# Performance work log

Hardware: AMD Instinct MI355X
Metric: run time of the kernel (lower is better)

The kernel has to match this reference:

```python
import jax, jax.numpy as jnp
import numpy as np

D_MODEL = 1024
N_HEADS = 16
DIM_HEAD = D_MODEL // N_HEADS
SCALE = DIM_HEAD ** -0.5


def setup_inputs() -> dict:
    key = jax.random.key(0)
    ks = jax.random.split(key, 7)
    B, N = 2, 2048
    q = jax.random.normal(ks[0], (B, N, D_MODEL), dtype=jnp.float32)
    # boolean mask: True = masked out; keep sparse so softmax rows stay valid
    mask = jax.random.bernoulli(ks[1], 0.1, (B, N, N))
    s = D_MODEL ** -0.5
    Wq = jax.random.normal(ks[2], (D_MODEL, D_MODEL), dtype=jnp.float32) * s
    Wk = jax.random.normal(ks[3], (D_MODEL, D_MODEL), dtype=jnp.float32) * s
    Wv = jax.random.normal(ks[4], (D_MODEL, D_MODEL), dtype=jnp.float32) * s
    Wo = jax.random.normal(ks[5], (D_MODEL, D_MODEL), dtype=jnp.float32) * s
    bo = jnp.zeros((D_MODEL,), dtype=jnp.float32)
    return {"q": q, "mask": mask, "Wq": Wq, "Wk": Wk, "Wv": Wv, "Wo": Wo, "bo": bo}


def reference(q, mask, Wq, Wk, Wv, Wo, bo):
    B, N, D = q.shape
    # self-attention: memory = q. nn.Linear applies x @ W.T (W is [out, in]).
    qh = (q @ Wq.T) * SCALE
    kh = q @ Wk.T
    vh = q @ Wv.T
    # b n (h d) -> b h n d
    qh = qh.reshape(B, N, N_HEADS, DIM_HEAD).transpose(0, 2, 1, 3)
    kh = kh.reshape(B, N, N_HEADS, DIM_HEAD).transpose(0, 2, 1, 3)
    vh = vh.reshape(B, N, N_HEADS, DIM_HEAD).transpose(0, 2, 1, 3)
    scores = jnp.einsum('bhid,bhjd->bhij', qh, kh)  # [B,H,N,N]
    mask_value = -jnp.finfo(scores.dtype).max
    scores = jnp.where(mask[:, None, :, :], mask_value, scores)
    attn = jax.nn.softmax(scores, axis=-1)
    o = jnp.einsum('bhij,bhjd->bhid', attn, vh)
    o = o.transpose(0, 2, 1, 3).reshape(B, N, D)  # b h n d -> b n (h d)
    return o @ Wo.T + bo
```

## Files before the change

kernel.cpp:

```cpp
#include <hip/hip_runtime.h>
#include <hip/hip_bf16.h>

typedef float fx4 __attribute__((ext_vector_type(4)));
typedef short s16x8 __attribute__((ext_vector_type(8)));

#define NSEQ 2048
#define DM   1024
#define NH   16
#define DH   64
#define MROWS 4096
#define NWORDS (2 * NSEQ * (NSEQ / 64))

#define QK_SCALE (0.125f * 1.44269504088896f)

__device__ __forceinline__ unsigned short f2bf(float f) {
    union { float f; unsigned u; } c; c.f = f;
    unsigned u = c.u;
    unsigned r = u + 0x7FFFu + ((u >> 16) & 1u);
    return (unsigned short)(r >> 16);
}

__device__ __forceinline__ float exp2_fast(float x) {
#if __has_builtin(__builtin_amdgcn_exp2f)
    return __builtin_amdgcn_exp2f(x);
#else
    return exp2f(x);
#endif
}

__device__ __forceinline__ unsigned cvt_pk_bf16(float a, float b) {
    unsigned r;
    asm("v_cvt_pk_bf16_f32 %0, %1, %2" : "=v"(r) : "v"(a), "v"(b));
    return r;
}

__device__ __forceinline__ fx4 zero4() {
    fx4 z; z[0] = 0.f; z[1] = 0.f; z[2] = 0.f; z[3] = 0.f; return z;
}

__device__ __forceinline__ void gload16(const void* g, void* l) {
    __builtin_amdgcn_global_load_lds(
        (const __attribute__((address_space(1))) unsigned int*)g,
        (__attribute__((address_space(3))) unsigned int*)l,
        16, 0, 0);
}

__global__ void cvt_kernel(const float* __restrict__ in,
                           unsigned short* __restrict__ out, int n4) {
    int i = blockIdx.x * blockDim.x + threadIdx.x;
    if (i >= n4) return;
    float4 v = reinterpret_cast<const float4*>(in)[i];
    ushort4 o;
    o.x = f2bf(v.x); o.y = f2bf(v.y); o.z = f2bf(v.z); o.w = f2bf(v.w);
    reinterpret_cast<ushort4*>(out)[i] = o;
}

__global__ void cvt4_kernel(const float* __restrict__ w0, const float* __restrict__ w1,
                            const float* __restrict__ w2, const float* __restrict__ w3,
                            unsigned short* __restrict__ o0, unsigned short* __restrict__ o1,
                            unsigned short* __restrict__ o2, unsigned short* __restrict__ o3) {
    const float* in; unsigned short* out;
    switch (blockIdx.y) {
        case 0:  in = w0; out = o0; break;
        case 1:  in = w1; out = o1; break;
        case 2:  in = w2; out = o2; break;
        default: in = w3; out = o3; break;
    }
    int i = blockIdx.x * blockDim.x + threadIdx.x;
    float4 v = reinterpret_cast<const float4*>(in)[i];
    ushort4 o;
    o.x = f2bf(v.x); o.y = f2bf(v.y); o.z = f2bf(v.z); o.w = f2bf(v.w);
    reinterpret_cast<ushort4*>(out)[i] = o;
}

__global__ void mask_detect(const unsigned int* __restrict__ m, int* __restrict__ flag) {
    unsigned mx = 0;
    int stride = gridDim.x * blockDim.x;
    for (int i = blockIdx.x * blockDim.x + threadIdx.x; i < (2 * NSEQ * NSEQ) / 4; i += stride) {
        unsigned v = m[i];
        mx = v > mx ? v : mx;
    }
    if (__any(mx > 1u)) {
        if ((threadIdx.x & 63) == 0) atomicOr(flag, 1);
    }
}

__global__ void mask_pack(const void* __restrict__ mask, const int* __restrict__ mflag,
                          unsigned long long* __restrict__ packed) {
    const int flg  = mflag[0];
    const int lane = threadIdx.x & 63;
    const int wpb  = blockDim.x >> 6;
    const int perm = ((lane >> 2) & 3) * 16 + ((lane >> 4) & 3) * 4 + (lane & 3);
    size_t w = (size_t)blockIdx.x * wpb + (threadIdx.x >> 6);
    const size_t stride = (size_t)gridDim.x * wpb;
    for (; w < NWORDS; w += stride) {
        size_t elem = (w >> 5) * (size_t)NSEQ + (size_t)(w & 31) * 64 + perm;
        int mv = flg ? (int)((const unsigned char*)mask)[elem]
                     : ((const int*)mask)[elem];
        unsigned long long bits = __ballot(mv != 0);
        if (lane == 0) packed[w] = bits;
    }
}

__global__ __launch_bounds__(256) void gemm_qkv(
        const unsigned short* __restrict__ A,
        const unsigned short* __restrict__ Wq,
        const unsigned short* __restrict__ Wk,
        const unsigned short* __restrict__ Wv,
        unsigned short* __restrict__ Qh,
        unsigned short* __restrict__ Kh,
        unsigned short* __restrict__ VhT) {
    __shared__ unsigned short As[128 * 32];
    __shared__ unsigned short Bs[128 * 32];

    const int tid  = threadIdx.x;
    const int lane = tid & 63;
    const int w    = tid >> 6;
    const int lr   = lane & 15;
    const int lg   = lane >> 4;
    const int wr   = (w >> 1) * 64;
    const int wc   = (w & 1) * 64;
    const int rowbase = blockIdx.y * 128;
    const int seg     = blockIdx.x >> 3;
    const int cb      = (blockIdx.x & 7) * 128;
    const unsigned short* W = seg == 0 ? Wq : (seg == 1 ? Wk : Wv);
    const float scale = seg == 0 ? QK_SCALE : 1.0f;

    fx4 acc[4][4];
#pragma unroll
    for (int i = 0; i < 4; i++)
#pragma unroll
        for (int j = 0; j < 4; j++) acc[i][j] = zero4();

    for (int k0 = 0; k0 < DM; k0 += 32) {
        __syncthreads();
#pragma unroll
        for (int i = 0; i < 2; i++) {
            int j = i * 256 + w * 64 + lane;
            int r = j >> 2, c8 = (j & 3) * 8;
            gload16(A + (size_t)(rowbase + r) * DM + k0 + c8,
                    As + (size_t)(i * 256 + w * 64) * 8);
            gload16(W + (size_t)(cb + r) * DM + k0 + c8,
                    Bs + (size_t)(i * 256 + w * 64) * 8);
        }
        __syncthreads();

        s16x8 af[4], bf[4];
#pragma unroll
        for (int mi = 0; mi < 4; mi++)
            af[mi] = *reinterpret_cast<const s16x8*>(&As[(wr + mi * 16 + lr) * 32 + 8 * lg]);
#pragma unroll
        for (int ni = 0; ni < 4; ni++)
            bf[ni] = *reinterpret_cast<const s16x8*>(&Bs[(wc + ni * 16 + lr) * 32 + 8 * lg]);
#pragma unroll
        for (int mi = 0; mi < 4; mi++)
#pragma unroll
            for (int ni = 0; ni < 4; ni++)
                acc[mi][ni] = __builtin_amdgcn_mfma_f32_16x16x32_bf16(af[mi], bf[ni], acc[mi][ni], 0, 0, 0);
    }

#pragma unroll
    for (int mi = 0; mi < 4; mi++) {
#pragma unroll
        for (int ni = 0; ni < 4; ni++) {
#pragma unroll
            for (int v = 0; v < 4; v++) {
                int m    = rowbase + wr + mi * 16 + lg * 4 + v;
                int cseg = cb + wc + ni * 16 + lr;
                float val = acc[mi][ni][v] * scale;
                int b = m >> 11, nseq = m & 2047;
                int h = cseg >> 6, dh = cseg & 63;
                if (seg < 2) {
                    unsigned short* dst = seg == 0 ? Qh : Kh;
                    dst[((size_t)(b * NH + h) * NSEQ + nseq) * DH + dh] = f2bf(val);
                } else {
                    VhT[((size_t)(b * NH + h) * DH + dh) * NSEQ + nseq] = f2bf(val);
                }
            }
        }
    }
}

__global__ __launch_bounds__(256) void gemm_out(
        const unsigned short* __restrict__ A,
        const unsigned short* __restrict__ W,
        float* __restrict__ out,
        const float* __restrict__ bias) {
    __shared__ unsigned short As[64 * 32];
    __shared__ unsigned short Bs[128 * 32];

    const int tid  = threadIdx.x;
    const int lane = tid & 63;
    const int w    = tid >> 6;
    const int lr   = lane & 15;
    const int lg   = lane >> 4;
    const int wr   = (w >> 1) * 32;
    const int wc   = (w & 1) * 64;
    const int rowbase = blockIdx.y * 64;
    const int colbase = blockIdx.x * 128;

    fx4 acc[2][4];
#pragma unroll
    for (int i = 0; i < 2; i++)
#pragma unroll
        for (int j = 0; j < 4; j++) acc[i][j] = zero4();

    for (int k0 = 0; k0 < DM; k0 += 32) {
        __syncthreads();
        {
            int j = tid;
            int r = j >> 2, c8 = (j & 3) * 8;
            gload16(A + (size_t)(rowbase + r) * DM + k0 + c8,
                    As + (size_t)(w * 64) * 8);
            gload16(W + (size_t)(colbase + r) * DM + k0 + c8,
                    Bs + (size_t)(w * 64) * 8);
            int r2 = 64 + (j >> 2);
            gload16(W + (size_t)(colbase + r2) * DM + k0 + c8,
                    Bs + (size_t)(256 + w * 64) * 8);
        }
        __syncthreads();

        s16x8 af[2], bf[4];
#pragma unroll
        for (int mi = 0; mi < 2; mi++)
            af[mi] = *reinterpret_cast<const s16x8*>(&As[(wr + mi * 16 + lr) * 32 + 8 * lg]);
#pragma unroll
        for (int ni = 0; ni < 4; ni++)
            bf[ni] = *reinterpret_cast<const s16x8*>(&Bs[(wc + ni * 16 + lr) * 32 + 8 * lg]);
#pragma unroll
        for (int mi = 0; mi < 2; mi++)
#pragma unroll
            for (int ni = 0; ni < 4; ni++)
                acc[mi][ni] = __builtin_amdgcn_mfma_f32_16x16x32_bf16(af[mi], bf[ni], acc[mi][ni], 0, 0, 0);
    }

#pragma unroll
    for (int mi = 0; mi < 2; mi++)
#pragma unroll
        for (int ni = 0; ni < 4; ni++)
#pragma unroll
            for (int v = 0; v < 4; v++) {
                int m = rowbase + wr + mi * 16 + lg * 4 + v;
                int c = colbase + wc + ni * 16 + lr;
                out[(size_t)m * DM + c] = acc[mi][ni][v] + bias[c];
            }
}

__global__ __launch_bounds__(256) void attn_kernel(
        const unsigned short* __restrict__ Qh,
        const unsigned short* __restrict__ Kh,
        const unsigned short* __restrict__ VhT,
        const unsigned long long* __restrict__ Mp,
        unsigned short* __restrict__ Obuf) {
    __shared__ unsigned short Ks[2][64 * 64];
    __shared__ unsigned short Vs[2][64 * 64];
    __shared__ __align__(16) unsigned int Ps[4][16 * 32];

    const int tid  = threadIdx.x;
    const int lane = tid & 63;
    const int w    = tid >> 6;
    const int lr   = lane & 15;
    const int lg   = lane >> 4;

    const int wg    = ((blockIdx.x & 7) << 7) + (blockIdx.x >> 3);
    const int qbase = (wg & 31) << 6;
    const int bh    = wg >> 5;
    const int b     = bh >> 4;
    const int h     = bh & 15;

    s16x8 qf[2];
    const size_t qrow = (size_t)bh * NSEQ + qbase + w * 16 + lr;
#pragma unroll
    for (int kk = 0; kk < 2; kk++)
        qf[kk] = *reinterpret_cast<const s16x8*>(Qh + qrow * DH + kk * 32 + 8 * lg);

    float mreg = -3.0e38f, lrow = 0.f;
    fx4 acc[4];
#pragma unroll
    for (int t = 0; t < 4; t++) acc[t] = zero4();

    const size_t mbase = ((size_t)b * NSEQ + qbase + w * 16 + lr) * (NSEQ / 64);

    auto stage = [&](int d, int kv0) {
#pragma unroll
        for (int i = 0; i < 2; i++) {
            int u  = i * 256 + w * 64 + lane;
            int r  = u >> 3, cs = u & 7;
            int cu = cs ^ (r & 7);
            gload16(Kh + ((size_t)bh * NSEQ + kv0 + r) * DH + cu * 8,
                    &Ks[d][(size_t)(i * 256 + w * 64) * 8]);
            gload16(VhT + ((size_t)bh * DH + r) * NSEQ + kv0 + cu * 8,
                    &Vs[d][(size_t)(i * 256 + w * 64) * 8]);
        }
    };

    stage(0, 0);
    __syncthreads();

    for (int it = 0; it < NSEQ / 64; it++) {
        const int cur = it & 1;
        if (it < NSEQ / 64 - 1) stage(cur ^ 1, (it + 1) << 6);

        unsigned long long pwm = Mp[mbase + it];
        unsigned mb = (unsigned)((pwm >> (lg * 16)) & 0xFFFFull);

        fx4 s[4];
        __builtin_amdgcn_s_setprio(1);
#pragma unroll
        for (int t = 0; t < 4; t++) {
            s[t] = zero4();
#pragma unroll
            for (int kk = 0; kk < 2; kk++) {
                int r  = t * 16 + lr;
                int cs = (kk * 4 + lg) ^ (r & 7);
                s16x8 kf = *reinterpret_cast<const s16x8*>(&Ks[cur][r * 64 + cs * 8]);
                s[t] = __builtin_amdgcn_mfma_f32_16x16x32_bf16(kf, qf[kk], s[t], 0, 0, 0);
            }
        }
        __builtin_amdgcn_s_setprio(0);

        float tmax = -3.0e38f;
#pragma unroll
        for (int t = 0; t < 4; t++)
#pragma unroll
            for (int v = 0; v < 4; v++) {
                float sv = (mb & (1u << (t * 4 + v))) ? -3.0e38f : s[t][v];
                s[t][v] = sv;
                tmax = fmaxf(tmax, sv);
            }
        tmax = fmaxf(tmax, __shfl_xor(tmax, 16));
        tmax = fmaxf(tmax, __shfl_xor(tmax, 32));

        if (__any(tmax > mreg + 8.0f)) {
            float mn = fmaxf(mreg, tmax);
            float sc = exp2_fast(mreg - mn);
            mreg = mn;
            lrow *= sc;
#pragma unroll
            for (int v = 0; v < 4; v++) {
                float scv = __shfl(sc, (lane & 48) | (lg * 4 + v));
#pragma unroll
                for (int t = 0; t < 4; t++) acc[t][v] *= scv;
            }
        }

        float psum = 0.f;
#pragma unroll
        for (int t = 0; t < 4; t++)
#pragma unroll
            for (int v = 0; v < 4; v++) {
                float p = exp2_fast(s[t][v] - mreg);
                s[t][v] = p;
                psum += p;
            }
        psum += __shfl_xor(psum, 16);
        psum += __shfl_xor(psum, 32);
        lrow += psum;

#pragma unroll
        for (int t = 0; t < 4; t++) {
            unsigned p0 = cvt_pk_bf16(s[t][0], s[t][1]);
            unsigned p1 = cvt_pk_bf16(s[t][2], s[t][3]);
            int idx = (t * 8 + lg * 2) ^ ((lr & 7) << 2);
            *reinterpret_cast<unsigned long long*>(&Ps[w][lr * 32 + idx]) =
                ((unsigned long long)p1 << 32) | p0;
        }

        __builtin_amdgcn_s_setprio(1);
#pragma unroll
        for (int kk = 0; kk < 2; kk++) {
            int ridx = (kk * 16 + lg * 4) ^ ((lr & 7) << 2);
            union { uint4 u; s16x8 v; } cvt;
            cvt.u = *reinterpret_cast<const uint4*>(&Ps[w][lr * 32 + ridx]);
            s16x8 pf = cvt.v;
#pragma unroll
            for (int t = 0; t < 4; t++) {
                int r  = t * 16 + lr;
                int cs = (kk * 4 + lg) ^ (r & 7);
                s16x8 vf = *reinterpret_cast<const s16x8*>(&Vs[cur][r * 64 + cs * 8]);
                acc[t] = __builtin_amdgcn_mfma_f32_16x16x32_bf16(pf, vf, acc[t], 0, 0, 0);
            }
        }
        __builtin_amdgcn_s_setprio(0);

        __syncthreads();
    }

#pragma unroll
    for (int v = 0; v < 4; v++) {
        float lq  = __shfl(lrow, (lane & 48) | (lg * 4 + v));
        float inv = 1.0f / lq;
        int q = qbase + w * 16 + lg * 4 + v;
#pragma unroll
        for (int t = 0; t < 4; t++) {
            int d = t * 16 + lr;
            Obuf[((size_t)b * NSEQ + q) * DM + h * DH + d] = f2bf(acc[t][v] * inv);
        }
    }
}

extern "C" void kernel_launch(void* const* d_in, const int* in_sizes, int n_in,
                              void* d_out, int out_size, void* d_ws, size_t ws_size,
                              hipStream_t stream) {
    const float* q    = (const float*)d_in[0];
    const void*  mask = (const void*)d_in[1];
    const float* Wq   = (const float*)d_in[2];
    const float* Wk   = (const float*)d_in[3];
    const float* Wv   = (const float*)d_in[4];
    const float* Wo   = (const float*)d_in[5];
    const float* bo   = (const float*)d_in[6];
    float* out = (float*)d_out;

    char* ws = (char*)d_ws;
    const size_t MB = 1024 * 1024;
    unsigned short* qbf  = (unsigned short*)(ws + 0);
    unsigned long long* packed = (unsigned long long*)(ws + 0);
    unsigned short* Wqb  = (unsigned short*)(ws + 8  * MB);
    unsigned short* Wkb  = (unsigned short*)(ws + 10 * MB);
    unsigned short* Wvb  = (unsigned short*)(ws + 12 * MB);
    unsigned short* Wob  = (unsigned short*)(ws + 14 * MB);
    unsigned short* Qh   = (unsigned short*)(ws + 16 * MB);
    unsigned short* Kh   = (unsigned short*)(ws + 24 * MB);
    unsigned short* VhT  = (unsigned short*)(ws + 32 * MB);
    unsigned short* Obuf = (unsigned short*)(ws + 40 * MB);
    int*            flag = (int*)(ws + 56 * MB);

    hipMemsetAsync(flag, 0, 4, stream);
    mask_detect<<<1024, 256, 0, stream>>>((const unsigned int*)mask, flag);

    cvt_kernel<<<4096, 256, 0, stream>>>(q, qbf, (2 * NSEQ * DM) / 4);
    cvt4_kernel<<<dim3(1024, 4), 256, 0, stream>>>(Wq, Wk, Wv, Wo, Wqb, Wkb, Wvb, Wob);

    gemm_qkv<<<dim3(24, 32), 256, 0, stream>>>(qbf, Wqb, Wkb, Wvb, Qh, Kh, VhT);

    mask_pack<<<1024, 256, 0, stream>>>(mask, flag, packed);

    attn_kernel<<<1024, 256, 0, stream>>>(Qh, Kh, VhT, packed, Obuf);

    gemm_out<<<dim3(8, 64), 256, 0, stream>>>(Obuf, Wob, out, bo);
}
```

Before: 254.4 us.

## Switch attention to 32x32x16 MFMA with 128-row query tiles and permlane P transfer

```diff
diff --git a/kernel.cpp b/kernel.cpp
--- a/kernel.cpp
+++ b/kernel.cpp
@@ -1,7 +1,8 @@
 #include <hip/hip_runtime.h>
 #include <hip/hip_bf16.h>
 
-typedef float fx4 __attribute__((ext_vector_type(4)));
+typedef float fx4  __attribute__((ext_vector_type(4)));
+typedef float fx16 __attribute__((ext_vector_type(16)));
 typedef short s16x8 __attribute__((ext_vector_type(8)));
 
 #define NSEQ 2048
@@ -36,6 +37,13 @@
 
 __device__ __forceinline__ fx4 zero4() {
     fx4 z; z[0] = 0.f; z[1] = 0.f; z[2] = 0.f; z[3] = 0.f; return z;
+}
+
+__device__ __forceinline__ fx16 zero16() {
+    fx16 z;
+#pragma unroll
+    for (int i = 0; i < 16; i++) z[i] = 0.f;
+    return z;
 }
 
 __device__ __forceinline__ void gload16(const void* g, void* l) {
@@ -90,7 +98,7 @@
     const int flg  = mflag[0];
     const int lane = threadIdx.x & 63;
     const int wpb  = blockDim.x >> 6;
-    const int perm = ((lane >> 2) & 3) * 16 + ((lane >> 4) & 3) * 4 + (lane & 3);
+    const int perm = (lane & 3) + 8 * ((lane >> 2) & 3) + 4 * (lane >> 5) + 32 * ((lane >> 4) & 1);
     size_t w = (size_t)blockIdx.x * wpb + (threadIdx.x >> 6);
     const size_t stride = (size_t)gridDim.x * wpb;
     for (; w < NWORDS; w += stride) {
@@ -254,32 +262,30 @@
         unsigned short* __restrict__ Obuf) {
     __shared__ unsigned short Ks[2][64 * 64];
     __shared__ unsigned short Vs[2][64 * 64];
-    __shared__ __align__(16) unsigned int Ps[4][16 * 32];
 
     const int tid  = threadIdx.x;
     const int lane = tid & 63;
     const int w    = tid >> 6;
-    const int lr   = lane & 15;
-    const int lg   = lane >> 4;
-
-    const int wg    = ((blockIdx.x & 7) << 7) + (blockIdx.x >> 3);
-    const int qbase = (wg & 31) << 6;
-    const int bh    = wg >> 5;
+    const int l31  = lane & 31;
+    const int hi   = lane >> 5;
+
+    const int wg    = ((blockIdx.x & 7) << 6) | (blockIdx.x >> 3);
+    const int qbase = (wg & 15) << 7;
+    const int bh    = wg >> 4;
     const int b     = bh >> 4;
     const int h     = bh & 15;
 
-    s16x8 qf[2];
-    const size_t qrow = (size_t)bh * NSEQ + qbase + w * 16 + lr;
-#pragma unroll
-    for (int kk = 0; kk < 2; kk++)
-        qf[kk] = *reinterpret_cast<const s16x8*>(Qh + qrow * DH + kk * 32 + 8 * lg);
+    s16x8 qf[4];
+    const size_t qrow = (size_t)bh * NSEQ + qbase + w * 32 + l31;
+#pragma unroll
+    for (int s = 0; s < 4; s++)
+        qf[s] = *reinterpret_cast<const s16x8*>(Qh + qrow * DH + s * 16 + hi * 8);
 
     float mreg = -3.0e38f, lrow = 0.f;
-    fx4 acc[4];
-#pragma unroll
-    for (int t = 0; t < 4; t++) acc[t] = zero4();
-
-    const size_t mbase = ((size_t)b * NSEQ + qbase + w * 16 + lr) * (NSEQ / 64);
+    fx16 po[2];
+    po[0] = zero16(); po[1] = zero16();
+
+    const size_t mbase = ((size_t)b * NSEQ + qbase + w * 32 + l31) * (NSEQ / 64);
 
     auto stage = [&](int d, int kv0) {
 #pragma unroll
@@ -302,33 +308,32 @@
         if (it < NSEQ / 64 - 1) stage(cur ^ 1, (it + 1) << 6);
 
         unsigned long long pwm = Mp[mbase + it];
-        unsigned mb = (unsigned)((pwm >> (lg * 16)) & 0xFFFFull);
-
-        fx4 s[4];
+        unsigned m32 = (unsigned)(pwm >> (hi * 32));
+
+        fx16 sx[2];
         __builtin_amdgcn_s_setprio(1);
 #pragma unroll
-        for (int t = 0; t < 4; t++) {
-            s[t] = zero4();
-#pragma unroll
-            for (int kk = 0; kk < 2; kk++) {
-                int r  = t * 16 + lr;
-                int cs = (kk * 4 + lg) ^ (r & 7);
+        for (int kh = 0; kh < 2; kh++) {
+            sx[kh] = zero16();
+            int r = kh * 32 + l31;
+#pragma unroll
+            for (int s = 0; s < 4; s++) {
+                int cs = (2 * s + hi) ^ (r & 7);
                 s16x8 kf = *reinterpret_cast<const s16x8*>(&Ks[cur][r * 64 + cs * 8]);
-                s[t] = __builtin_amdgcn_mfma_f32_16x16x32_bf16(kf, qf[kk], s[t], 0, 0, 0);
+                sx[kh] = __builtin_amdgcn_mfma_f32_32x32x16_bf16(kf, qf[s], sx[kh], 0, 0, 0);
             }
         }
         __builtin_amdgcn_s_setprio(0);
 
         float tmax = -3.0e38f;
 #pragma unroll
-        for (int t = 0; t < 4; t++)
-#pragma unroll
-            for (int v = 0; v < 4; v++) {
-                float sv = (mb & (1u << (t * 4 + v))) ? -3.0e38f : s[t][v];
-                s[t][v] = sv;
+        for (int kh = 0; kh < 2; kh++)
+#pragma unroll
+            for (int reg = 0; reg < 16; reg++) {
+                float sv = (m32 & (1u << (kh * 16 + reg))) ? -3.0e38f : sx[kh][reg];
+                sx[kh][reg] = sv;
                 tmax = fmaxf(tmax, sv);
             }
-        tmax = fmaxf(tmax, __shfl_xor(tmax, 16));
         tmax = fmaxf(tmax, __shfl_xor(tmax, 32));
 
         if (__any(tmax > mreg + 8.0f)) {
@@ -337,48 +342,44 @@
             mreg = mn;
             lrow *= sc;
 #pragma unroll
-            for (int v = 0; v < 4; v++) {
-                float scv = __shfl(sc, (lane & 48) | (lg * 4 + v));
-#pragma unroll
-                for (int t = 0; t < 4; t++) acc[t][v] *= scv;
+            for (int reg = 0; reg < 16; reg++) {
+                int qr = (reg & 3) + 8 * (reg >> 2) + 4 * hi;
+                float scq = __shfl(sc, qr);
+                po[0][reg] *= scq;
+                po[1][reg] *= scq;
             }
         }
 
         float psum = 0.f;
 #pragma unroll
-        for (int t = 0; t < 4; t++)
-#pragma unroll
-            for (int v = 0; v < 4; v++) {
-                float p = exp2_fast(s[t][v] - mreg);
-                s[t][v] = p;
+        for (int kh = 0; kh < 2; kh++)
+#pragma unroll
+            for (int reg = 0; reg < 16; reg++) {
+                float p = exp2_fast(sx[kh][reg] - mreg);
+                sx[kh][reg] = p;
                 psum += p;
             }
-        psum += __shfl_xor(psum, 16);
         psum += __shfl_xor(psum, 32);
         lrow += psum;
 
-#pragma unroll
-        for (int t = 0; t < 4; t++) {
-            unsigned p0 = cvt_pk_bf16(s[t][0], s[t][1]);
-            unsigned p1 = cvt_pk_bf16(s[t][2], s[t][3]);
-            int idx = (t * 8 + lg * 2) ^ ((lr & 7) << 2);
-            *reinterpret_cast<unsigned long long*>(&Ps[w][lr * 32 + idx]) =
-                ((unsigned long long)p1 << 32) | p0;
-        }
-
         __builtin_amdgcn_s_setprio(1);
 #pragma unroll
-        for (int kk = 0; kk < 2; kk++) {
-            int ridx = (kk * 16 + lg * 4) ^ ((lr & 7) << 2);
-            union { uint4 u; s16x8 v; } cvt;
-            cvt.u = *reinterpret_cast<const uint4*>(&Ps[w][lr * 32 + ridx]);
-            s16x8 pf = cvt.v;
-#pragma unroll
-            for (int t = 0; t < 4; t++) {
-                int r  = t * 16 + lr;
-                int cs = (kk * 4 + lg) ^ (r & 7);
+        for (int ks = 0; ks < 4; ks++) {
+            const int kh = ks >> 1, rb = (ks & 1) * 8;
+            unsigned o0w0 = cvt_pk_bf16(sx[kh][rb + 0], sx[kh][rb + 1]);
+            unsigned o0w1 = cvt_pk_bf16(sx[kh][rb + 2], sx[kh][rb + 3]);
+            unsigned o1w0 = cvt_pk_bf16(sx[kh][rb + 4], sx[kh][rb + 5]);
+            unsigned o1w1 = cvt_pk_bf16(sx[kh][rb + 6], sx[kh][rb + 7]);
+            asm("v_permlane32_swap_b32 %0, %1" : "+v"(o0w0), "+v"(o1w0));
+            asm("v_permlane32_swap_b32 %0, %1" : "+v"(o0w1), "+v"(o1w1));
+            union { unsigned u[4]; s16x8 v; } pk;
+            pk.u[0] = o0w0; pk.u[1] = o0w1; pk.u[2] = o1w0; pk.u[3] = o1w1;
+#pragma unroll
+            for (int dt = 0; dt < 2; dt++) {
+                int r  = dt * 32 + l31;
+                int cs = (2 * ks + hi) ^ (r & 7);
                 s16x8 vf = *reinterpret_cast<const s16x8*>(&Vs[cur][r * 64 + cs * 8]);
-                acc[t] = __builtin_amdgcn_mfma_f32_16x16x32_bf16(pf, vf, acc[t], 0, 0, 0);
+                po[dt] = __builtin_amdgcn_mfma_f32_32x32x16_bf16(pk.v, vf, po[dt], 0, 0, 0);
             }
         }
         __builtin_amdgcn_s_setprio(0);
@@ -386,15 +387,16 @@
         __syncthreads();
     }
 
-#pragma unroll
-    for (int v = 0; v < 4; v++) {
-        float lq  = __shfl(lrow, (lane & 48) | (lg * 4 + v));
-        float inv = 1.0f / lq;
-        int q = qbase + w * 16 + lg * 4 + v;
-#pragma unroll
-        for (int t = 0; t < 4; t++) {
-            int d = t * 16 + lr;
-            Obuf[((size_t)b * NSEQ + q) * DM + h * DH + d] = f2bf(acc[t][v] * inv);
+    float inv = 1.0f / lrow;
+#pragma unroll
+    for (int reg = 0; reg < 16; reg++) {
+        int qr = (reg & 3) + 8 * (reg >> 2) + 4 * hi;
+        float invq = __shfl(inv, qr);
+        int q = qbase + w * 32 + qr;
+#pragma unroll
+        for (int dt = 0; dt < 2; dt++) {
+            int d = dt * 32 + l31;
+            Obuf[((size_t)b * NSEQ + q) * DM + h * DH + d] = f2bf(po[dt][reg] * invq);
         }
     }
 }
@@ -435,7 +437,7 @@
 
     mask_pack<<<1024, 256, 0, stream>>>(mask, flag, packed);
 
-    attn_kernel<<<1024, 256, 0, stream>>>(Qh, Kh, VhT, packed, Obuf);
+    attn_kernel<<<512, 256, 0, stream>>>(Qh, Kh, VhT, packed, Obuf);
 
     gemm_out<<<dim3(8, 64), 256, 0, stream>>>(Obuf, Wob, out, bo);
 }
```

Result: no change. 253.9 us (-0.2%).
